# Performance work log

Measured on AMD Instinct MI355X. Metric: run time of the kernel, lower is better.

Reference implementation:

```python
import jax, jax.numpy as jnp
import numpy as np

N_ATOMS = 256
N_FEATURES = 128
BATCH = 8
BINS = 300


def _segments(n, length=1):
    # all pairs of non-overlapping length-`length` segments: rows [i, i+L, j, j+L], j >= i+L+1
    m = n - length
    i, j = np.triu_indices(m, k=length + 1)
    return np.stack([i, i + length, j, j + length], axis=1).astype(np.int32)  # (Nseg, 4)


SEGMENTS_NP = _segments(N_ATOMS)
NSEG = SEGMENTS_NP.shape[0]  # 32131 for n_atoms=256
# edges: segment start-pairs and end-pairs, shape (2, 2*Nseg), then offset per frame
_edges_base = np.concatenate([SEGMENTS_NP[:, [0, 2]], SEGMENTS_NP[:, [1, 3]]], axis=0).T
EDGES_NP = np.concatenate([b * N_ATOMS + _edges_base for b in range(BATCH)], axis=1)  # (2, B*2*Nseg)
SRC = jnp.asarray(EDGES_NP[0].astype(np.int32))
DST = jnp.asarray(EDGES_NP[1].astype(np.int32))
SEGMENTS = jnp.asarray(SEGMENTS_NP)
BIN_CENTERS = jnp.linspace(-1.0, 1.0, BINS, dtype=jnp.float32)
STEP = 2.0 / (BINS - 1)  # linear (non-gaussian) binning: scalar step


def _divnorm(x):
    return x / jnp.linalg.norm(x, axis=-1, keepdims=True)


def _writhe_segments_cross(xyz, seg):
    # xyz: (B, N, 3), seg: (S, 4) -> writhe per segment pair (B, S)
    B, S = xyz.shape[0], seg.shape[0]
    # dx[b, s, k]: broadcasted differences xyz[seg[2+q]] - xyz[seg[p]], k = 2*p+q
    dx = (-xyz[:, seg[:, :2], None] + xyz[:, seg[:, None, 2:]]).reshape(B, S, 4, 3)
    dx = _divnorm(dx)
    crosses = _divnorm(jnp.cross(dx[:, :, [0, 1, 3, 2]], dx[:, :, [1, 3, 2, 0]]))
    dots = jnp.clip(jnp.sum(crosses * crosses[:, :, [1, 2, 3, 0]], axis=-1), -1.0, 1.0)
    omega = jnp.arcsin(dots).sum(axis=2)  # (B, S)
    signs = jnp.sign(jnp.sum(
        jnp.cross(xyz[:, seg[:, 3]] - xyz[:, seg[:, 2]], xyz[:, seg[:, 1]] - xyz[:, seg[:, 0]]) * dx[:, :, 0],
        axis=-1))
    return omega * signs / (2.0 * jnp.pi)


def setup_inputs() -> dict:
    key = jax.random.key(0)
    k1, k2, k3 = jax.random.split(key, 3)
    coords = jax.random.normal(k1, (BATCH * N_ATOMS, 3), jnp.float32)
    node_features = jax.random.normal(k2, (BATCH * N_ATOMS, N_FEATURES), jnp.float32)
    std = 1.0 / np.sqrt(N_FEATURES)
    basis = jax.random.uniform(k3, (BINS, N_FEATURES), jnp.float32, -std, std)
    return {"coords": coords, "node_features": node_features, "basis": basis}


def reference(coords, node_features, basis):
    xyz = coords.reshape(BATCH, N_ATOMS, 3)
    wr = _writhe_segments_cross(xyz, SEGMENTS)  # (B, Nseg)
    # Gaussian RBF soft one-hot over linear bins, then project onto learned basis
    enc = jnp.exp(-(((wr[..., None] - BIN_CENTERS) / STEP) ** 2)) / 1.12  # (B, S, bins)
    emb = jnp.einsum('bsk,kf->bsf', enc, basis)  # (B, S, F)
    # repeat(1,2,1): each segment pair contributes two edges (start-pair, end-pair)
    writhe_feat = jnp.tile(emb, (1, 2, 1)).reshape(-1, N_FEATURES)  # (B*2S, F)
    # distance attention: exp(-||r_src - r_dst||^2), softmax-normalized per destination node
    w = jnp.exp(-jnp.sum((coords[SRC] - coords[DST]) ** 2, axis=-1))  # (E,)
    denom = jax.ops.segment_sum(w, DST, num_segments=BATCH * N_ATOMS)
    attn = (w / denom[DST])[:, None]
    message = jax.ops.segment_sum(writhe_feat * attn, DST, num_segments=BATCH * N_ATOMS)
    return node_features + message
```

## Files before the change

kernel.cpp:

```cpp
#include <hip/hip_runtime.h>
#include <math.h>

#define N_ATOMS 256
#define N_FEAT  128
#define BATCH   8
#define BINS    300
#define INV_STEP 149.5f
#define ONE_OVER_2PI 0.15915494309189535f
#define INV_112 0.8928571428571429f
#define WIN 2
#define WINW 5
#define NHIST 4
#define EXPM2 0.13533528323661270f

struct V3 { float x, y, z; };
__device__ __forceinline__ V3 v3sub(V3 a, V3 b) { return {a.x-b.x, a.y-b.y, a.z-b.z}; }
__device__ __forceinline__ float v3dot(V3 a, V3 b) { return a.x*b.x + a.y*b.y + a.z*b.z; }
__device__ __forceinline__ V3 v3cross(V3 a, V3 b) {
    return {a.y*b.z - a.z*b.y, a.z*b.x - a.x*b.z, a.x*b.y - a.y*b.x};
}
__device__ __forceinline__ float clamp1(float x) { return fminf(1.0f, fmaxf(-1.0f, x)); }

__device__ __forceinline__ float asin_fast(float x) {
    float u = fabsf(x);
    bool big = u > 0.5f;
    float z = big ? 0.5f * (1.0f - u) : u * u;
    float s = big ? __builtin_amdgcn_sqrtf(z) : u;
    float p = fmaf(z, 4.2163199048e-2f, 2.4181311049e-2f);
    p = fmaf(z, p, 4.5470025998e-2f);
    p = fmaf(z, p, 7.4953002686e-2f);
    p = fmaf(z, p, 1.6666752422e-1f);
    float r = fmaf(s * z, p, s);
    r = big ? (1.5707963267948966f - 2.0f * r) : r;
    return copysignf(r, x);
}

__device__ __forceinline__ float writhe_ij(const float4* cs, int i, int j) {
    const float4 qi  = cs[i],   qi1 = cs[i + 1];
    const float4 qj  = cs[j],   qj1 = cs[j + 1];
    V3 pi  = {qi.x,  qi.y,  qi.z};
    V3 pi1 = {qi1.x, qi1.y, qi1.z};
    V3 pj  = {qj.x,  qj.y,  qj.z};
    V3 pj1 = {qj1.x, qj1.y, qj1.z};

    V3 u0 = v3sub(pj,  pi);
    V3 u1 = v3sub(pj1, pi);
    V3 u2 = v3sub(pj,  pi1);
    V3 u3 = v3sub(pj1, pi1);

    V3 c0 = v3cross(u0, u1);
    V3 c1 = v3cross(u1, u3);
    V3 c2 = v3cross(u3, u2);
    V3 c3 = v3cross(u2, u0);

    float r0 = __builtin_amdgcn_rsqf(v3dot(c0, c0));
    float r1 = __builtin_amdgcn_rsqf(v3dot(c1, c1));
    float r2 = __builtin_amdgcn_rsqf(v3dot(c2, c2));
    float r3 = __builtin_amdgcn_rsqf(v3dot(c3, c3));

    float omega = asin_fast(clamp1(v3dot(c0, c1) * (r0 * r1)))
                + asin_fast(clamp1(v3dot(c1, c2) * (r1 * r2)))
                + asin_fast(clamp1(v3dot(c2, c3) * (r2 * r3)))
                + asin_fast(clamp1(v3dot(c3, c0) * (r3 * r0)));

    float sg = v3dot(v3cross(v3sub(pj1, pj), v3sub(pi1, pi)), u0);
    float sign = (sg > 0.0f) ? 1.0f : ((sg < 0.0f) ? -1.0f : 0.0f);
    return omega * sign * ONE_OVER_2PI;
}

__device__ __forceinline__ void edge_compute(const float4* cs, int tau, int ee,
                                             float& g, float& pp, int& k0) {
    const int eT1 = (tau <= N_ATOMS - 2) ? tau - 1 : 0;
    const int typ = (ee < eT1) ? 0 : 1;
    const int a = (typ == 0) ? ee : ee - eT1 + 1;

    const float4 qa = cs[a];
    const float4 qt = cs[tau];
    const float dx = qa.x - qt.x;
    const float dy = qa.y - qt.y;
    const float dz = qa.z - qt.z;
    g = __expf(-(dx*dx + dy*dy + dz*dz));

    const float w = writhe_ij(cs, a - typ, tau - typ);
    pp = (w + 1.0f) * INV_STEP;
    k0 = __float2int_rn(pp);
}

__global__ __launch_bounds__(256) void fused_kernel(const float* __restrict__ coords,
                                                    const float* __restrict__ nf,
                                                    const float* __restrict__ basis,
                                                    float* __restrict__ out) {
    const int blk = blockIdx.x;
    const int b = blk & 7;
    const int p = blk >> 3;
    const int t0 = p + 2;
    const int t1 = 255 - p;
    const int tid = threadIdx.x;

    const int E0  = 2 * t0 - 3;
    const int E1n = (t1 == 255) ? 253 : 2 * t1 - 3;
    const int E = E0 + E1n;

    const int nu_out = tid >> 7;
    const int f_out = tid & 127;
    const int row_out = nu_out ? t1 : t0;
    const float mynf = nf[((size_t)((b << 8) | row_out)) * N_FEAT + f_out];

    __shared__ float4 cs[N_ATOMS];
    __shared__ float h2[2 * NHIST * BINS];
    __shared__ float sden[2];
    __shared__ int skmin[2], skmax[2];

    {
        const int gbase = ((b << 8) + tid) * 3;
        cs[tid] = make_float4(coords[gbase], coords[gbase + 1], coords[gbase + 2], 0.0f);
    }
    if (tid < 2) { sden[tid] = 0.0f; skmin[tid] = BINS - 1; skmax[tid] = 0; }
    __syncthreads();

    const bool act1 = (tid < E);
    const int node1e = (tid < E0) ? 0 : 1;
    const int ee1 = (node1e == 1) ? min(tid - E0, E1n - 1) : tid;
    const int tau1 = node1e ? t1 : t0;

    const bool act2 = (tid + 256 < E);
    const int ee2 = act2 ? (tid + 256 - E0) : 0;

    float g1, pp1; int k01;
    float g2, pp2; int k02;
    edge_compute(cs, tau1, ee1, g1, pp1, k01);
    edge_compute(cs, t1,   ee2, g2, pp2, k02);

    float d0 = (act1 && node1e == 0) ? g1 : 0.0f;
    float d1 = ((act1 && node1e == 1) ? g1 : 0.0f) + (act2 ? g2 : 0.0f);
    int kn0 = BINS - 1, kx0 = 0, kn1 = BINS - 1, kx1 = 0;
    if (act1) {
        const int kmn = max(0, k01 - WIN), kmx = min(BINS - 1, k01 + WIN);
        if (node1e == 0) { kn0 = kmn; kx0 = kmx; } else { kn1 = kmn; kx1 = kmx; }
    }
    if (act2) {
        kn1 = min(kn1, max(0, k02 - WIN));
        kx1 = max(kx1, min(BINS - 1, k02 + WIN));
    }

    #pragma unroll
    for (int off = 32; off > 0; off >>= 1) {
        d0 += __shfl_xor(d0, off, 64);
        d1 += __shfl_xor(d1, off, 64);
        kn0 = min(kn0, __shfl_xor(kn0, off, 64));
        kx0 = max(kx0, __shfl_xor(kx0, off, 64));
        kn1 = min(kn1, __shfl_xor(kn1, off, 64));
        kx1 = max(kx1, __shfl_xor(kx1, off, 64));
    }
    if ((tid & 63) == 0) {
        atomicAdd(&sden[0], d0);
        atomicAdd(&sden[1], d1);
        atomicMin(&skmin[0], kn0);
        atomicMax(&skmax[0], kx0);
        atomicMin(&skmin[1], kn1);
        atomicMax(&skmax[1], kx1);
    }
    __syncthreads();

    {
        const int nu = tid >> 7;
        const int l = tid & 127;
        const int kmin = skmin[nu], kmax = skmax[nu];
        const int base = nu * NHIST * BINS;
        for (int k = kmin + l; k <= kmax; k += 128) {
            #pragma unroll
            for (int c = 0; c < NHIST; ++c) h2[base + c * BINS + k] = 0.0f;
        }
    }
    __syncthreads();

    const int copy = tid & (NHIST - 1);
    if (act1) {
        const int base = (node1e * NHIST + copy) * BINS;
        const int klo = k01 - WIN;
        float d = pp1 - (float)klo;
        float e = g1 * __expf(-d * d);
        float u = __expf(2.0f * d - 1.0f);
        #pragma unroll
        for (int m = 0; m < WINW; ++m) {
            const int k = klo + m;
            if (k >= 0 && k < BINS) atomicAdd(&h2[base + k], e);
            e *= u;
            u *= EXPM2;
        }
    }
    if (act2) {
        const int base = (NHIST + copy) * BINS;
        const int klo = k02 - WIN;
        float d = pp2 - (float)klo;
        float e = g2 * __expf(-d * d);
        float u = __expf(2.0f * d - 1.0f);
        #pragma unroll
        for (int m = 0; m < WINW; ++m) {
            const int k = klo + m;
            if (k >= 0 && k < BINS) atomicAdd(&h2[base + k], e);
            e *= u;
            u *= EXPM2;
        }
    }
    __syncthreads();

    {
        const int nu = tid >> 7;
        const int kmin = skmin[nu], kmax = skmax[nu];
        const int base = nu * NHIST * BINS;
        for (int k = kmin + (tid & 127); k <= kmax; k += 128) {
            h2[base + k] = h2[base + k] + h2[base + BINS + k]
                         + h2[base + 2 * BINS + k] + h2[base + 3 * BINS + k];
        }
    }
    __syncthreads();

    {
        const int kmin = skmin[nu_out], kmax = skmax[nu_out];
        const int base = nu_out * NHIST * BINS;
        float acc0 = 0.0f, acc1 = 0.0f;
        int k = kmin;
        for (; k + 1 <= kmax; k += 2) {
            acc0 = fmaf(h2[base + k],     basis[k * N_FEAT + f_out],       acc0);
            acc1 = fmaf(h2[base + k + 1], basis[(k + 1) * N_FEAT + f_out], acc1);
        }
        if (k <= kmax) acc0 = fmaf(h2[base + k], basis[k * N_FEAT + f_out], acc0);
        out[((size_t)((b << 8) | row_out)) * N_FEAT + f_out]
            = mynf + (acc0 + acc1) * (INV_112 / sden[nu_out]);
    }
    if (p == 0) {
        const size_t idx = ((size_t)((b << 8) | nu_out)) * N_FEAT + f_out;
        out[idx] = nf[idx];
    }
}

extern "C" void kernel_launch(void* const* d_in, const int* in_sizes, int n_in,
                              void* d_out, int out_size, void* d_ws, size_t ws_size,
                              hipStream_t stream) {
    const float* coords = (const float*)d_in[0];
    const float* nf     = (const float*)d_in[1];
    const float* basis  = (const float*)d_in[2];
    float* out = (float*)d_out;

    fused_kernel<<<BATCH * 127, 256, 0, stream>>>(coords, nf, basis, out);
}
```

Baseline: 99.33 us.

## Halve block size to 128 threads, each handling four edges and both output rows

The block shrinks from 256 to 128 threads. Each thread now computes four edges instead of two and produces the projection for both destination rows, looping over the two histograms. The aim is to cut idle lanes, since E is at most about 510, and to give more work per thread, but it doubles the serial projection loop per thread. It may also lower latency hiding because fewer threads per block share the same LDS footprint.

Measured after the change: 149.6 us. 1.51x slower.

```diff
diff --git a/kernel.cpp b/kernel.cpp
--- a/kernel.cpp
+++ b/kernel.cpp
@@ -86,7 +86,21 @@
     k0 = __float2int_rn(pp);
 }
 
-__global__ __launch_bounds__(256) void fused_kernel(const float* __restrict__ coords,
+__device__ __forceinline__ void deposit(float* h2, int base, float g, float pp, int k0) {
+    const int klo = k0 - WIN;
+    float d = pp - (float)klo;
+    float e = g * __expf(-d * d);
+    float u = __expf(2.0f * d - 1.0f);
+    #pragma unroll
+    for (int m = 0; m < WINW; ++m) {
+        const int k = klo + m;
+        if (k >= 0 && k < BINS) atomicAdd(&h2[base + k], e);
+        e *= u;
+        u *= EXPM2;
+    }
+}
+
+__global__ __launch_bounds__(128) void fused_kernel(const float* __restrict__ coords,
                                                     const float* __restrict__ nf,
                                                     const float* __restrict__ basis,
                                                     float* __restrict__ out) {
@@ -101,10 +115,8 @@
     const int E1n = (t1 == 255) ? 253 : 2 * t1 - 3;
     const int E = E0 + E1n;
 
-    const int nu_out = tid >> 7;
-    const int f_out = tid & 127;
-    const int row_out = nu_out ? t1 : t0;
-    const float mynf = nf[((size_t)((b << 8) | row_out)) * N_FEAT + f_out];
+    const float mynf0 = nf[((size_t)((b << 8) | t0)) * N_FEAT + tid];
+    const float mynf1 = nf[((size_t)((b << 8) | t1)) * N_FEAT + tid];
 
     __shared__ float4 cs[N_ATOMS];
     __shared__ float h2[2 * NHIST * BINS];
@@ -112,36 +124,47 @@
     __shared__ int skmin[2], skmax[2];
 
     {
-        const int gbase = ((b << 8) + tid) * 3;
-        cs[tid] = make_float4(coords[gbase], coords[gbase + 1], coords[gbase + 2], 0.0f);
+        const int g0 = ((b << 8) + tid) * 3;
+        const int g1 = ((b << 8) + tid + 128) * 3;
+        cs[tid]       = make_float4(coords[g0], coords[g0 + 1], coords[g0 + 2], 0.0f);
+        cs[tid + 128] = make_float4(coords[g1], coords[g1 + 1], coords[g1 + 2], 0.0f);
     }
     if (tid < 2) { sden[tid] = 0.0f; skmin[tid] = BINS - 1; skmax[tid] = 0; }
     __syncthreads();
 
-    const bool act1 = (tid < E);
-    const int node1e = (tid < E0) ? 0 : 1;
-    const int ee1 = (node1e == 1) ? min(tid - E0, E1n - 1) : tid;
-    const int tau1 = node1e ? t1 : t0;
-
-    const bool act2 = (tid + 256 < E);
-    const int ee2 = act2 ? (tid + 256 - E0) : 0;
-
-    float g1, pp1; int k01;
-    float g2, pp2; int k02;
-    edge_compute(cs, tau1, ee1, g1, pp1, k01);
-    edge_compute(cs, t1,   ee2, g2, pp2, k02);
-
-    float d0 = (act1 && node1e == 0) ? g1 : 0.0f;
-    float d1 = ((act1 && node1e == 1) ? g1 : 0.0f) + (act2 ? g2 : 0.0f);
+    const int e1 = tid, e2 = tid + 128, e3 = tid + 256, e4 = tid + 384;
+    const bool a1 = (e1 < E), a2 = (e2 < E), a3 = (e3 < E), a4 = (e4 < E);
+    const int n1 = (e1 < E0) ? 0 : 1;
+    const int n2 = (e2 < E0) ? 0 : 1;
+    const int ee1 = n1 ? min(e1 - E0, E1n - 1) : e1;
+    const int ee2 = n2 ? min(e2 - E0, E1n - 1) : e2;
+    const int ee3 = min(e3 - E0, E1n - 1);
+    const int ee4 = min(e4 - E0, E1n - 1);
+
+    float g1v, pp1; int k01;
+    float g2v, pp2; int k02;
+    float g3v, pp3; int k03;
+    float g4v, pp4; int k04;
+    edge_compute(cs, n1 ? t1 : t0, ee1, g1v, pp1, k01);
+    edge_compute(cs, n2 ? t1 : t0, ee2, g2v, pp2, k02);
+    edge_compute(cs, t1, ee3, g3v, pp3, k03);
+    edge_compute(cs, t1, ee4, g4v, pp4, k04);
+
+    float d0 = ((a1 && n1 == 0) ? g1v : 0.0f) + ((a2 && n2 == 0) ? g2v : 0.0f);
+    float d1 = ((a1 && n1 == 1) ? g1v : 0.0f) + ((a2 && n2 == 1) ? g2v : 0.0f)
+             + (a3 ? g3v : 0.0f) + (a4 ? g4v : 0.0f);
     int kn0 = BINS - 1, kx0 = 0, kn1 = BINS - 1, kx1 = 0;
-    if (act1) {
+    if (a1) {
         const int kmn = max(0, k01 - WIN), kmx = min(BINS - 1, k01 + WIN);
-        if (node1e == 0) { kn0 = kmn; kx0 = kmx; } else { kn1 = kmn; kx1 = kmx; }
-    }
-    if (act2) {
-        kn1 = min(kn1, max(0, k02 - WIN));
-        kx1 = max(kx1, min(BINS - 1, k02 + WIN));
-    }
+        if (n1 == 0) { kn0 = kmn; kx0 = kmx; } else { kn1 = kmn; kx1 = kmx; }
+    }
+    if (a2) {
+        const int kmn = max(0, k02 - WIN), kmx = min(BINS - 1, k02 + WIN);
+        if (n2 == 0) { kn0 = min(kn0, kmn); kx0 = max(kx0, kmx); }
+        else         { kn1 = min(kn1, kmn); kx1 = max(kx1, kmx); }
+    }
+    if (a3) { kn1 = min(kn1, max(0, k03 - WIN)); kx1 = max(kx1, min(BINS - 1, k03 + WIN)); }
+    if (a4) { kn1 = min(kn1, max(0, k04 - WIN)); kx1 = max(kx1, min(BINS - 1, k04 + WIN)); }
 
     #pragma unroll
     for (int off = 32; off > 0; off >>= 1) {
@@ -163,11 +186,11 @@
     __syncthreads();
 
     {
-        const int nu = tid >> 7;
-        const int l = tid & 127;
+        const int nu = tid >> 6;
+        const int l = tid & 63;
         const int kmin = skmin[nu], kmax = skmax[nu];
         const int base = nu * NHIST * BINS;
-        for (int k = kmin + l; k <= kmax; k += 128) {
+        for (int k = kmin + l; k <= kmax; k += 64) {
             #pragma unroll
             for (int c = 0; c < NHIST; ++c) h2[base + c * BINS + k] = 0.0f;
         }
@@ -175,41 +198,17 @@
     __syncthreads();
 
     const int copy = tid & (NHIST - 1);
-    if (act1) {
-        const int base = (node1e * NHIST + copy) * BINS;
-        const int klo = k01 - WIN;
-        float d = pp1 - (float)klo;
-        float e = g1 * __expf(-d * d);
-        float u = __expf(2.0f * d - 1.0f);
-        #pragma unroll
-        for (int m = 0; m < WINW; ++m) {
-            const int k = klo + m;
-            if (k >= 0 && k < BINS) atomicAdd(&h2[base + k], e);
-            e *= u;
-            u *= EXPM2;
-        }
-    }
-    if (act2) {
-        const int base = (NHIST + copy) * BINS;
-        const int klo = k02 - WIN;
-        float d = pp2 - (float)klo;
-        float e = g2 * __expf(-d * d);
-        float u = __expf(2.0f * d - 1.0f);
-        #pragma unroll
-        for (int m = 0; m < WINW; ++m) {
-            const int k = klo + m;
-            if (k >= 0 && k < BINS) atomicAdd(&h2[base + k], e);
-            e *= u;
-            u *= EXPM2;
-        }
-    }
-    __syncthreads();
-
-    {
-        const int nu = tid >> 7;
+    if (a1) deposit(h2, (n1 * NHIST + copy) * BINS, g1v, pp1, k01);
+    if (a2) deposit(h2, (n2 * NHIST + copy) * BINS, g2v, pp2, k02);
+    if (a3) deposit(h2, (NHIST + copy) * BINS, g3v, pp3, k03);
+    if (a4) deposit(h2, (NHIST + copy) * BINS, g4v, pp4, k04);
+    __syncthreads();
+
+    {
+        const int nu = tid >> 6;
         const int kmin = skmin[nu], kmax = skmax[nu];
         const int base = nu * NHIST * BINS;
-        for (int k = kmin + (tid & 127); k <= kmax; k += 128) {
+        for (int k = kmin + (tid & 63); k <= kmax; k += 64) {
             h2[base + k] = h2[base + k] + h2[base + BINS + k]
                          + h2[base + 2 * BINS + k] + h2[base + 3 * BINS + k];
         }
@@ -217,21 +216,26 @@
     __syncthreads();
 
     {
-        const int kmin = skmin[nu_out], kmax = skmax[nu_out];
-        const int base = nu_out * NHIST * BINS;
         float acc0 = 0.0f, acc1 = 0.0f;
-        int k = kmin;
-        for (; k + 1 <= kmax; k += 2) {
-            acc0 = fmaf(h2[base + k],     basis[k * N_FEAT + f_out],       acc0);
-            acc1 = fmaf(h2[base + k + 1], basis[(k + 1) * N_FEAT + f_out], acc1);
-        }
-        if (k <= kmax) acc0 = fmaf(h2[base + k], basis[k * N_FEAT + f_out], acc0);
-        out[((size_t)((b << 8) | row_out)) * N_FEAT + f_out]
-            = mynf + (acc0 + acc1) * (INV_112 / sden[nu_out]);
+        {
+            const int kmin = skmin[0], kmax = skmax[0];
+            for (int k = kmin; k <= kmax; ++k)
+                acc0 = fmaf(h2[k], basis[k * N_FEAT + tid], acc0);
+        }
+        {
+            const int kmin = skmin[1], kmax = skmax[1];
+            const int base = NHIST * BINS;
+            for (int k = kmin; k <= kmax; ++k)
+                acc1 = fmaf(h2[base + k], basis[k * N_FEAT + tid], acc1);
+        }
+        out[((size_t)((b << 8) | t0)) * N_FEAT + tid] = mynf0 + acc0 * (INV_112 / sden[0]);
+        out[((size_t)((b << 8) | t1)) * N_FEAT + tid] = mynf1 + acc1 * (INV_112 / sden[1]);
     }
     if (p == 0) {
-        const size_t idx = ((size_t)((b << 8) | nu_out)) * N_FEAT + f_out;
-        out[idx] = nf[idx];
+        const size_t i0 = ((size_t)(b << 8)) * N_FEAT + tid;
+        const size_t i1 = ((size_t)((b << 8) | 1)) * N_FEAT + tid;
+        out[i0] = nf[i0];
+        out[i1] = nf[i1];
     }
 }
 
@@ -243,5 +247,5 @@
     const float* basis  = (const float*)d_in[2];
     float* out = (float*)d_out;
 
-    fused_kernel<<<BATCH * 127, 256, 0, stream>>>(coords, nf, basis, out);
-}
+    fused_kernel<<<BATCH * 127, 128, 0, stream>>>(coords, nf, basis, out);
+}
```
